# Kernel tuning notes

Measured on AMD Instinct MI355X. Metric: run time of the kernel, lower is better.

## Reference

```python
import jax, jax.numpy as jnp
import numpy as np

NUM_HEADS = 16
DIM_HEAD = 64
MAX_LEN = 512


def setup_inputs() -> dict:
    key = jax.random.key(0)
    ks = jax.random.split(key, 6)
    B, N, D = 16, 512, 1024
    inner = NUM_HEADS * DIM_HEAD  # 1024
    x = jax.random.normal(ks[0], (B, N, D), dtype=jnp.float32)
    w_qkv = jax.random.normal(ks[1], (D, 3 * inner), dtype=jnp.float32) * (D ** -0.5)
    b_qkv = jnp.zeros((3 * inner,), dtype=jnp.float32)
    rel_emb = jax.random.normal(ks[2], (2 * MAX_LEN - 1, NUM_HEADS), dtype=jnp.float32) * 0.02
    w_out = jax.random.normal(ks[3], (inner, D), dtype=jnp.float32) * (inner ** -0.5)
    b_out = jnp.zeros((D,), dtype=jnp.float32)
    return {"x": x, "w_qkv": w_qkv, "b_qkv": b_qkv, "rel_emb": rel_emb,
            "w_out": w_out, "b_out": b_out}


def reference(x, w_qkv, b_qkv, rel_emb, w_out, b_out):
    B, N, D = x.shape
    h, dh = NUM_HEADS, DIM_HEAD
    scale = dh ** -0.5
    qkv = x @ w_qkv + b_qkv  # (B, N, 3*h*dh)
    q, k, v = jnp.split(qkv, 3, axis=-1)
    def to_heads(t):
        return t.reshape(B, N, h, dh).transpose(0, 2, 1, 3)  # (B, h, N, dh)
    q, k, v = to_heads(q), to_heads(k), to_heads(v)
    dots = jnp.einsum('bhid,bhjd->bhij', q, k) * scale  # (B, h, N, N)
    # relative position bias: emb[(i - j) + max_len - 1] -> (N, N, h) -> (1, h, N, N)
    idx = jnp.arange(N)[:, None] - jnp.arange(N)[None, :] + (MAX_LEN - 1)
    bias = rel_emb[idx].transpose(2, 0, 1)[None]  # (1, h, N, N)
    attn = jax.nn.softmax(dots + bias, axis=-1)
    out = jnp.einsum('bhij,bhjd->bhid', attn, v)  # (B, h, N, dh)
    out = out.transpose(0, 2, 1, 3).reshape(B, N, h * dh)
    return out @ w_out + b_out
```

## Files before the change

### kernel.cpp

```cpp
#include <hip/hip_runtime.h>

#define SEQ    512
#define NH     16
#define DH     64
#define DMODEL 1024
#define NB     16
#define MROWS  (NB*SEQ)
#define MAXL   512

typedef _Float16 f16;
typedef f16  f16x8 __attribute__((ext_vector_type(8)));
typedef f16  f16x4 __attribute__((ext_vector_type(4)));
typedef float f32x4 __attribute__((ext_vector_type(4)));

__device__ static inline void gll16(const f16* g, f16* l) {
    __builtin_amdgcn_global_load_lds(
        (const __attribute__((address_space(1))) void*)(g),
        (__attribute__((address_space(3))) void*)(l), 16, 0, 0);
}

__global__ __launch_bounds__(256)
void prep(const float* __restrict__ x, f16* __restrict__ xh,
          const float* __restrict__ wqkv, f16* __restrict__ wqkvT,
          const float* __restrict__ wout, f16* __restrict__ woutT)
{
    const int bid = blockIdx.x, t = threadIdx.x;
    if (bid < 8192) {
        int i = (bid * 256 + t) * 4;
        float4 v = *(const float4*)(x + i);
        f16x4 h = { (f16)v.x, (f16)v.y, (f16)v.z, (f16)v.w };
        *(f16x4*)(xh + i) = h;
        return;
    }
    __shared__ float tile[32][33];
    const float* in; f16* out; int C, gx, gy;
    if (bid < 8192 + 3072) {
        int b2 = bid - 8192; in = wqkv; out = wqkvT; C = 3072;
        gx = b2 % 96; gy = b2 / 96;
    } else {
        int b2 = bid - 11264; in = wout; out = woutT; C = 1024;
        gx = b2 & 31; gy = b2 >> 5;
    }
    const int R = 1024;
    int tx = t & 31, ty = t >> 5;
    int c0 = gx * 32, r0 = gy * 32;
    #pragma unroll
    for (int i = 0; i < 4; ++i)
        tile[ty + i * 8][tx] = in[(size_t)(r0 + ty + i * 8) * C + c0 + tx];
    __syncthreads();
    #pragma unroll
    for (int i = 0; i < 4; ++i)
        out[(size_t)(c0 + ty + i * 8) * R + r0 + tx] = (f16)tile[tx][ty + i * 8];
}

template<int MODE>
__global__ __launch_bounds__(256)
void gemm_mfma(const f16* __restrict__ A, const f16* __restrict__ Bt,
               const float* __restrict__ bias, int N, int K,
               float* __restrict__ Cout,
               f16* __restrict__ qb, f16* __restrict__ kb, f16* __restrict__ vb)
{
    __shared__ f16 As[128 * 64];
    __shared__ f16 Bs[128 * 64];
    const int t = threadIdx.x;
    const int lane = t & 63, w = t >> 6;
    const int quad = lane >> 4, l16 = lane & 15;
    const int xr = l16 & 7;
    const int m0 = blockIdx.y * 128, n0 = blockIdx.x * 128;
    const int wm = (w & 1) * 64, wn = (w >> 1) * 64;

    f32x4 acc[4][4];
    #pragma unroll
    for (int i = 0; i < 4; ++i)
        #pragma unroll
        for (int j = 0; j < 4; ++j)
            acc[i][j] = f32x4{0.f, 0.f, 0.f, 0.f};

    const int sr8 = lane >> 3;
    const int sc8 = (lane & 7) ^ sr8;
    const f16* agp = A  + (size_t)(m0 + w * 32 + sr8) * K + sc8 * 8;
    const f16* bgp = Bt + (size_t)(n0 + w * 32 + sr8) * K + sc8 * 8;
    f16* asl = As + w * 2048;
    f16* bsl = Bs + w * 2048;

    for (int k0 = 0; k0 < K; k0 += 64) {
        __syncthreads();
        #pragma unroll
        for (int c = 0; c < 4; ++c) {
            gll16(agp + k0 + c * 8 * K, asl + c * 512);
            gll16(bgp + k0 + c * 8 * K, bsl + c * 512);
        }
        __syncthreads();
        #pragma unroll
        for (int ks = 0; ks < 2; ++ks) {
            f16x8 af[4], bf[4];
            #pragma unroll
            for (int ms = 0; ms < 4; ++ms)
                af[ms] = *(const f16x8*)&As[(wm + ms * 16 + l16) * 64
                                            + (((ks * 4 + quad) ^ xr) * 8)];
            #pragma unroll
            for (int ns = 0; ns < 4; ++ns)
                bf[ns] = *(const f16x8*)&Bs[(wn + ns * 16 + l16) * 64
                                            + (((ks * 4 + quad) ^ xr) * 8)];
            #pragma unroll
            for (int ms = 0; ms < 4; ++ms)
                #pragma unroll
                for (int ns = 0; ns < 4; ++ns)
                    acc[ms][ns] = __builtin_amdgcn_mfma_f32_16x16x32_f16(
                        af[ms], bf[ns], acc[ms][ns], 0, 0, 0);
        }
    }

    if (MODE == 0) {
        #pragma unroll
        for (int ns = 0; ns < 4; ++ns) {
            int col = n0 + wn + ns * 16 + l16;
            float bv = bias[col];
            int which = col >> 10;
            int hh = (col & 1023) >> 6, d = col & 63;
            #pragma unroll
            for (int ms = 0; ms < 4; ++ms) {
                int rowb = m0 + wm + ms * 16 + quad * 4;
                int bb_ = rowb >> 9, n_ = rowb & 511;
                if (which == 0) {
                    f16x4 pk;
                    #pragma unroll
                    for (int reg = 0; reg < 4; ++reg)
                        pk[reg] = (f16)(acc[ms][ns][reg] + bv);
                    *(f16x4*)(qb + ((size_t)(bb_ * NH + hh) * DH + d) * SEQ + n_) = pk;
                } else if (which == 2) {
                    f16x4 pk;
                    #pragma unroll
                    for (int reg = 0; reg < 4; ++reg)
                        pk[reg] = (f16)(acc[ms][ns][reg] + bv);
                    int c8s = ((n_ >> 3) & 7) ^ (d & 7);
                    *(f16x4*)(vb + ((size_t)(bb_ * NH + hh) * DH + d) * SEQ
                                 + (n_ & ~63) + c8s * 8 + (n_ & 7)) = pk;
                } else {
                    #pragma unroll
                    for (int reg = 0; reg < 4; ++reg) {
                        int n = n_ + reg;
                        int dd = (((d >> 3) ^ (n & 7)) * 8) + (d & 7);
                        kb[((size_t)(bb_ * NH + hh) * SEQ + n) * DH + dd] =
                            (f16)(acc[ms][ns][reg] + bv);
                    }
                }
            }
        }
    } else {
        #pragma unroll
        for (int ns = 0; ns < 4; ++ns) {
            int col = n0 + wn + ns * 16 + l16;
            float bv = bias[col];
            #pragma unroll
            for (int ms = 0; ms < 4; ++ms) {
                int rowb = m0 + wm + ms * 16 + quad * 4;
                #pragma unroll
                for (int reg = 0; reg < 4; ++reg)
                    Cout[(size_t)(rowb + reg) * N + col] = acc[ms][ns][reg] + bv;
            }
        }
    }
}

__global__ __launch_bounds__(256)
void attn_mfma(const f16* __restrict__ qb, const f16* __restrict__ kb,
               const f16* __restrict__ vb, const float* __restrict__ rel,
               f16* __restrict__ ob)
{
    __shared__ f16 Ks[64 * 64];
    __shared__ f16 Vt[64 * 64];
    __shared__ f16 Pw[4][16 * 64];
    __shared__ float relh[1024];

    const int t = threadIdx.x;
    const int lane = t & 63, w = t >> 6;
    const int quad = lane >> 4, l16 = lane & 15;
    const int bid = blockIdx.x;
    const int bh = bid & 255, qt = bid >> 8;
    const int h = bh & 15, b = bh >> 4;

    for (int i = t; i < 2 * MAXL - 1; i += 256)
        relh[i] = rel[i * NH + h] * 1.44269504f;

    const f16* qbase = qb + (size_t)bh * DH * SEQ + (qt * 64 + w * 16 + l16);
    f16x8 qf0, qf1;
    #pragma unroll
    for (int j = 0; j < 8; ++j) {
        qf0[j] = qbase[(quad * 8 + j) * SEQ];
        qf1[j] = qbase[(quad * 8 + j + 32) * SEQ];
    }

    f32x4 o[4];
    #pragma unroll
    for (int dt = 0; dt < 4; ++dt) o[dt] = f32x4{0.f, 0.f, 0.f, 0.f};
    float lsum = 0.f;

    const f16* kpl = kb + (size_t)bh * SEQ * DH
                   + (size_t)(w * 16 + (lane >> 3)) * DH + (lane & 7) * 8;
    const f16* vpl = vb + (size_t)bh * DH * SEQ
                   + (size_t)(w * 16 + (lane >> 3)) * SEQ + (lane & 7) * 8;
    f16* kdst = Ks + w * 1024;
    f16* vdst = Vt + w * 1024;

    const int xr = l16 & 7;
    const int i0 = qt * 64 + w * 16 + l16;

    for (int kt = 0; kt < 8; ++kt) {
        __syncthreads();
        gll16(kpl + kt * 64 * DH,          kdst);
        gll16(kpl + kt * 64 * DH + 8 * DH, kdst + 512);
        gll16(vpl + kt * 64,               vdst);
        gll16(vpl + kt * 64 + 8 * SEQ,     vdst + 512);
        __syncthreads();

        f32x4 sT[4];
        #pragma unroll
        for (int mt = 0; mt < 4; ++mt) {
            const f16* kr = &Ks[(mt * 16 + l16) * 64];
            f16x8 a0 = *(const f16x8*)(kr + ((quad ^ xr) * 8));
            f16x8 a1 = *(const f16x8*)(kr + (((4 + quad) ^ xr) * 8));
            f32x4 c = f32x4{0.f, 0.f, 0.f, 0.f};
            c = __builtin_amdgcn_mfma_f32_16x16x32_f16(a0, qf0, c, 0, 0, 0);
            c = __builtin_amdgcn_mfma_f32_16x16x32_f16(a1, qf1, c, 0, 0, 0);
            sT[mt] = c;
        }

        const int cbase = i0 + (MAXL - 1) - kt * 64 - quad * 4;
        f16* pw = &Pw[w][0];
        #pragma unroll
        for (int mt = 0; mt < 4; ++mt) {
            f16x4 pk;
            #pragma unroll
            for (int reg = 0; reg < 4; ++reg) {
                float e = exp2f(fmaf(sT[mt][reg], 0.180336878f,
                                     relh[cbase - mt * 16 - reg]));
                lsum += e;
                pk[reg] = (f16)e;
            }
            int c8 = (mt * 2 + (quad >> 1)) ^ xr;
            *(f16x4*)&pw[l16 * 64 + c8 * 8 + (quad & 1) * 4] = pk;
        }
        __builtin_amdgcn_s_waitcnt(0xC07F);

        #pragma unroll
        for (int s2 = 0; s2 < 2; ++s2) {
            f16x8 pa = *(const f16x8*)&pw[l16 * 64 + (((s2 * 4 + quad) ^ xr) * 8)];
            #pragma unroll
            for (int dt = 0; dt < 4; ++dt) {
                const f16* vr = &Vt[(dt * 16 + l16) * 64];
                f16x8 vb8 = *(const f16x8*)(vr + (((s2 * 4 + quad) ^ xr) * 8));
                o[dt] = __builtin_amdgcn_mfma_f32_16x16x32_f16(pa, vb8, o[dt], 0, 0, 0);
            }
        }
    }

    lsum += __shfl_xor(lsum, 16, 64);
    lsum += __shfl_xor(lsum, 32, 64);
    #pragma unroll
    for (int reg = 0; reg < 4; ++reg) {
        float inv = 1.0f / __shfl(lsum, quad * 4 + reg, 64);
        size_t rbase = ((size_t)b * SEQ + qt * 64 + w * 16 + quad * 4 + reg) * DMODEL
                     + h * DH;
        #pragma unroll
        for (int dt = 0; dt < 4; ++dt)
            ob[rbase + dt * 16 + l16] = (f16)(o[dt][reg] * inv);
    }
}

extern "C" void kernel_launch(void* const* d_in, const int* in_sizes, int n_in,
                              void* d_out, int out_size, void* d_ws, size_t ws_size,
                              hipStream_t stream)
{
    const float* x    = (const float*)d_in[0];
    const float* wqkv = (const float*)d_in[1];
    const float* bqkv = (const float*)d_in[2];
    const float* rel  = (const float*)d_in[3];
    const float* wout = (const float*)d_in[4];
    const float* bout = (const float*)d_in[5];
    float* out = (float*)d_out;
    char* ws = (char*)d_ws;

    const size_t XH = (size_t)MROWS * DMODEL;
    f16* xh    = (f16*)(ws);
    f16* wqkvT = (f16*)(ws + 2 * XH);
    f16* woutT = wqkvT + (size_t)3 * DMODEL * DMODEL;
    f16* qbuf  = woutT + (size_t)DMODEL * DMODEL;
    f16* kbuf  = qbuf + XH;
    f16* vbuf  = kbuf + XH;
    f16* abuf  = vbuf + XH;

    prep<<<12288, 256, 0, stream>>>(x, xh, wqkv, wqkvT, wout, woutT);

    gemm_mfma<0><<<dim3(3 * DMODEL / 128, MROWS / 128), 256, 0, stream>>>(
        xh, wqkvT, bqkv, 3 * DMODEL, DMODEL, nullptr, qbuf, kbuf, vbuf);

    attn_mfma<<<dim3(NB * NH * (SEQ / 64)), 256, 0, stream>>>(
        qbuf, kbuf, vbuf, rel, abuf);

    gemm_mfma<1><<<dim3(DMODEL / 128, MROWS / 128), 256, 0, stream>>>(
        abuf, woutT, bout, DMODEL, DMODEL, out, nullptr, nullptr, nullptr);
}
```

Baseline: 239.5 us.

## Process whole sequence per (batch,head) block with 512 threads and 128-key tiles

The attention kernel now launches one 512-thread block per batch-head instead of eight 64-query blocks. Each wave handles 64 queries in four 16-row chunks, and K/V tiles grow to 128 keys. This cuts redundant K/V loads and relh table setup, since each head's K/V is now loaded once instead of eight times. The Q buffer layout also changes to row-major [bh][n][d], so Q fragments can be read with vector loads; the GEMM epilogue now writes scalar f16 stores for Q. The trade-offs are fewer blocks (256) for the GPU, much higher register pressure from 16 accumulators per wave, and larger shared memory use.

```diff
diff --git a/kernel.cpp b/kernel.cpp
--- a/kernel.cpp
+++ b/kernel.cpp
@@ -123,11 +123,10 @@
                 int rowb = m0 + wm + ms * 16 + quad * 4;
                 int bb_ = rowb >> 9, n_ = rowb & 511;
                 if (which == 0) {
-                    f16x4 pk;
                     #pragma unroll
                     for (int reg = 0; reg < 4; ++reg)
-                        pk[reg] = (f16)(acc[ms][ns][reg] + bv);
-                    *(f16x4*)(qb + ((size_t)(bb_ * NH + hh) * DH + d) * SEQ + n_) = pk;
+                        qb[((size_t)(bb_ * NH + hh) * SEQ + n_ + reg) * DH + d] =
+                            (f16)(acc[ms][ns][reg] + bv);
                 } else if (which == 2) {
                     f16x4 pk;
                     #pragma unroll
@@ -163,108 +162,125 @@
     }
 }
 
-__global__ __launch_bounds__(256)
+__global__ __launch_bounds__(512)
 void attn_mfma(const f16* __restrict__ qb, const f16* __restrict__ kb,
                const f16* __restrict__ vb, const float* __restrict__ rel,
                f16* __restrict__ ob)
 {
-    __shared__ f16 Ks[64 * 64];
-    __shared__ f16 Vt[64 * 64];
-    __shared__ f16 Pw[4][16 * 64];
+    __shared__ f16 Ks[128 * 64];
+    __shared__ f16 Vt[64 * 128];
+    __shared__ f16 Pw[8][16 * 64];
     __shared__ float relh[1024];
 
     const int t = threadIdx.x;
     const int lane = t & 63, w = t >> 6;
     const int quad = lane >> 4, l16 = lane & 15;
-    const int bid = blockIdx.x;
-    const int bh = bid & 255, qt = bid >> 8;
+    const int xr = l16 & 7;
+    const int bh = blockIdx.x;
     const int h = bh & 15, b = bh >> 4;
 
-    for (int i = t; i < 2 * MAXL - 1; i += 256)
+    for (int i = t; i < 2 * MAXL - 1; i += 512)
         relh[i] = rel[i * NH + h] * 1.44269504f;
 
-    const f16* qbase = qb + (size_t)bh * DH * SEQ + (qt * 64 + w * 16 + l16);
-    f16x8 qf0, qf1;
-    #pragma unroll
-    for (int j = 0; j < 8; ++j) {
-        qf0[j] = qbase[(quad * 8 + j) * SEQ];
-        qf1[j] = qbase[(quad * 8 + j + 32) * SEQ];
-    }
-
-    f32x4 o[4];
-    #pragma unroll
-    for (int dt = 0; dt < 4; ++dt) o[dt] = f32x4{0.f, 0.f, 0.f, 0.f};
-    float lsum = 0.f;
-
-    const f16* kpl = kb + (size_t)bh * SEQ * DH
-                   + (size_t)(w * 16 + (lane >> 3)) * DH + (lane & 7) * 8;
-    const f16* vpl = vb + (size_t)bh * DH * SEQ
-                   + (size_t)(w * 16 + (lane >> 3)) * SEQ + (lane & 7) * 8;
-    f16* kdst = Ks + w * 1024;
-    f16* vdst = Vt + w * 1024;
-
-    const int xr = l16 & 7;
-    const int i0 = qt * 64 + w * 16 + l16;
-
-    for (int kt = 0; kt < 8; ++kt) {
+    f16x8 qf[4][2];
+    #pragma unroll
+    for (int c = 0; c < 4; ++c) {
+        const f16* qrow = qb + ((size_t)bh * SEQ + w * 64 + c * 16 + l16) * DH + quad * 8;
+        qf[c][0] = *(const f16x8*)(qrow);
+        qf[c][1] = *(const f16x8*)(qrow + 32);
+    }
+
+    f32x4 o[4][4];
+    float lsum[4];
+    #pragma unroll
+    for (int c = 0; c < 4; ++c) {
+        lsum[c] = 0.f;
+        #pragma unroll
+        for (int dt = 0; dt < 4; ++dt) o[c][dt] = f32x4{0.f, 0.f, 0.f, 0.f};
+    }
+
+    const f16* kbase = kb + (size_t)bh * SEQ * DH;
+    const f16* vbase = vb + (size_t)bh * DH * SEQ;
+    f16* pw = &Pw[w][0];
+
+    for (int kt = 0; kt < 4; ++kt) {
         __syncthreads();
-        gll16(kpl + kt * 64 * DH,          kdst);
-        gll16(kpl + kt * 64 * DH + 8 * DH, kdst + 512);
-        gll16(vpl + kt * 64,               vdst);
-        gll16(vpl + kt * 64 + 8 * SEQ,     vdst + 512);
+        #pragma unroll
+        for (int r = 0; r < 2; ++r) {
+            const f16* src = kbase + (size_t)(kt * 128 + r * 64 + w * 8 + (lane >> 3)) * DH
+                           + (lane & 7) * 8;
+            gll16(src, Ks + r * 4096 + w * 512);
+        }
+        #pragma unroll
+        for (int r = 0; r < 2; ++r) {
+            const f16* src = vbase + (size_t)(r * 32 + w * 4 + (lane >> 4)) * SEQ
+                           + kt * 128 + ((lane & 15) >> 3) * 64 + (lane & 7) * 8;
+            gll16(src, Vt + r * 4096 + w * 512);
+        }
         __syncthreads();
 
-        f32x4 sT[4];
-        #pragma unroll
-        for (int mt = 0; mt < 4; ++mt) {
-            const f16* kr = &Ks[(mt * 16 + l16) * 64];
-            f16x8 a0 = *(const f16x8*)(kr + ((quad ^ xr) * 8));
-            f16x8 a1 = *(const f16x8*)(kr + (((4 + quad) ^ xr) * 8));
-            f32x4 c = f32x4{0.f, 0.f, 0.f, 0.f};
-            c = __builtin_amdgcn_mfma_f32_16x16x32_f16(a0, qf0, c, 0, 0, 0);
-            c = __builtin_amdgcn_mfma_f32_16x16x32_f16(a1, qf1, c, 0, 0, 0);
-            sT[mt] = c;
-        }
-
-        const int cbase = i0 + (MAXL - 1) - kt * 64 - quad * 4;
-        f16* pw = &Pw[w][0];
-        #pragma unroll
-        for (int mt = 0; mt < 4; ++mt) {
-            f16x4 pk;
-            #pragma unroll
-            for (int reg = 0; reg < 4; ++reg) {
-                float e = exp2f(fmaf(sT[mt][reg], 0.180336878f,
-                                     relh[cbase - mt * 16 - reg]));
-                lsum += e;
-                pk[reg] = (f16)e;
+        #pragma unroll
+        for (int c = 0; c < 4; ++c) {
+            f32x4 sT[8];
+            #pragma unroll
+            for (int mt = 0; mt < 8; ++mt) {
+                const f16* kr = &Ks[(mt * 16 + l16) * 64];
+                f16x8 a0 = *(const f16x8*)(kr + ((quad ^ xr) * 8));
+                f16x8 a1 = *(const f16x8*)(kr + (((4 + quad) ^ xr) * 8));
+                f32x4 s = f32x4{0.f, 0.f, 0.f, 0.f};
+                s = __builtin_amdgcn_mfma_f32_16x16x32_f16(a0, qf[c][0], s, 0, 0, 0);
+                s = __builtin_amdgcn_mfma_f32_16x16x32_f16(a1, qf[c][1], s, 0, 0, 0);
+                sT[mt] = s;
             }
-            int c8 = (mt * 2 + (quad >> 1)) ^ xr;
-            *(f16x4*)&pw[l16 * 64 + c8 * 8 + (quad & 1) * 4] = pk;
-        }
-        __builtin_amdgcn_s_waitcnt(0xC07F);
-
-        #pragma unroll
-        for (int s2 = 0; s2 < 2; ++s2) {
-            f16x8 pa = *(const f16x8*)&pw[l16 * 64 + (((s2 * 4 + quad) ^ xr) * 8)];
-            #pragma unroll
-            for (int dt = 0; dt < 4; ++dt) {
-                const f16* vr = &Vt[(dt * 16 + l16) * 64];
-                f16x8 vb8 = *(const f16x8*)(vr + (((s2 * 4 + quad) ^ xr) * 8));
-                o[dt] = __builtin_amdgcn_mfma_f32_16x16x32_f16(pa, vb8, o[dt], 0, 0, 0);
+
+            const int cb0 = w * 64 + c * 16 + l16 + (MAXL - 1) - kt * 128 - quad * 4;
+            #pragma unroll
+            for (int g = 0; g < 2; ++g) {
+                #pragma unroll
+                for (int m4 = 0; m4 < 4; ++m4) {
+                    int mt = g * 4 + m4;
+                    f16x4 pk;
+                    #pragma unroll
+                    for (int reg = 0; reg < 4; ++reg) {
+                        float e = exp2f(fmaf(sT[mt][reg], 0.180336878f,
+                                             relh[cb0 - mt * 16 - reg]));
+                        lsum[c] += e;
+                        pk[reg] = (f16)e;
+                    }
+                    int c8 = (m4 * 2 + (quad >> 1)) ^ xr;
+                    *(f16x4*)&pw[l16 * 64 + c8 * 8 + (quad & 1) * 4] = pk;
+                }
+                __builtin_amdgcn_s_waitcnt(0xC07F);
+
+                #pragma unroll
+                for (int s2 = 0; s2 < 2; ++s2) {
+                    f16x8 pa = *(const f16x8*)&pw[l16 * 64 + (((s2 * 4 + quad) ^ xr) * 8)];
+                    #pragma unroll
+                    for (int dt = 0; dt < 4; ++dt) {
+                        const f16* vr = &Vt[(dt * 16 + l16) * 128 + g * 64];
+                        f16x8 vb8 = *(const f16x8*)(vr + (((s2 * 4 + quad) ^ xr) * 8));
+                        o[c][dt] = __builtin_amdgcn_mfma_f32_16x16x32_f16(
+                            pa, vb8, o[c][dt], 0, 0, 0);
+                    }
+                }
             }
         }
     }
 
-    lsum += __shfl_xor(lsum, 16, 64);
-    lsum += __shfl_xor(lsum, 32, 64);
-    #pragma unroll
-    for (int reg = 0; reg < 4; ++reg) {
-        float inv = 1.0f / __shfl(lsum, quad * 4 + reg, 64);
-        size_t rbase = ((size_t)b * SEQ + qt * 64 + w * 16 + quad * 4 + reg) * DMODEL
-                     + h * DH;
-        #pragma unroll
-        for (int dt = 0; dt < 4; ++dt)
-            ob[rbase + dt * 16 + l16] = (f16)(o[dt][reg] * inv);
+    #pragma unroll
+    for (int c = 0; c < 4; ++c) {
+        float ls = lsum[c];
+        ls += __shfl_xor(ls, 16, 64);
+        ls += __shfl_xor(ls, 32, 64);
+        #pragma unroll
+        for (int reg = 0; reg < 4; ++reg) {
+            float inv = 1.0f / __shfl(ls, quad * 4 + reg, 64);
+            size_t rbase = ((size_t)b * SEQ + w * 64 + c * 16 + quad * 4 + reg) * DMODEL
+                         + h * DH;
+            #pragma unroll
+            for (int dt = 0; dt < 4; ++dt)
+                ob[rbase + dt * 16 + l16] = (f16)(o[c][dt][reg] * inv);
+        }
     }
 }
 
@@ -295,8 +311,7 @@
     gemm_mfma<0><<<dim3(3 * DMODEL / 128, MROWS / 128), 256, 0, stream>>>(
         xh, wqkvT, bqkv, 3 * DMODEL, DMODEL, nullptr, qbuf, kbuf, vbuf);
 
-    attn_mfma<<<dim3(NB * NH * (SEQ / 64)), 256, 0, stream>>>(
-        qbuf, kbuf, vbuf, rel, abuf);
+    attn_mfma<<<NB * NH, 512, 0, stream>>>(qbuf, kbuf, vbuf, rel, abuf);
 
     gemm_mfma<1><<<dim3(DMODEL / 128, MROWS / 128), 256, 0, stream>>>(
         abuf, woutT, bout, DMODEL, DMODEL, out, nullptr, nullptr, nullptr);
```

Result: faster. 230.1 us (-3.9%).
